# Optimization experiments

Measured on AMD Instinct MI355X. Metric: run time of the kernel, lower is better.

## Reference

```python
import jax, jax.numpy as jnp
import numpy as np

B, T, E, H, N_TAGS = 128, 512, 256, 512, 32
START, END = 30, 31


def setup_inputs() -> dict:
    key = jax.random.key(0)
    ks = jax.random.split(key, 12)
    s = 1.0 / np.sqrt(H)

    def w(k, shape):
        return jax.random.normal(k, shape, jnp.float32) * s

    X = jax.random.normal(ks[0], (B, T, E), jnp.float32)
    length = jnp.sort(jax.random.randint(ks[1], (B,), T // 2, T + 1))[::-1]
    masks = (jnp.arange(T)[None, :] < length[:, None]).astype(jnp.float32)
    W_ih_f, W_hh_f, b_f = w(ks[2], (4 * H, E)), w(ks[3], (4 * H, H)), w(ks[4], (4 * H,))
    W_ih_b, W_hh_b, b_b = w(ks[5], (4 * H, E)), w(ks[6], (4 * H, H)), w(ks[7], (4 * H,))
    W_out, b_out = w(ks[8], (N_TAGS, 2 * H)), w(ks[9], (N_TAGS,))
    transitions = jax.random.normal(ks[10], (N_TAGS, N_TAGS), jnp.float32)
    transitions = transitions.at[:, START].set(-1e4).at[END, :].set(-1e4)
    return dict(X=X, masks=masks, length=length,
                W_ih_f=W_ih_f, W_hh_f=W_hh_f, b_f=b_f,
                W_ih_b=W_ih_b, W_hh_b=W_hh_b, b_b=b_b,
                W_out=W_out, b_out=b_out, transitions=transitions)


def _lstm_dir(Xt, mt, Wih, Whh, b, reverse):
    # Xt: [T,B,E], mt: [T,B,1]. Masked update emulates pack_padded_sequence
    # (state frozen on pad; for reverse dir, state stays zero until last valid token).
    h0 = jnp.zeros((Xt.shape[1], H), Xt.dtype)

    def step(carry, inp):
        h, c = carry
        x, m = inp
        gates = x @ Wih.T + h @ Whh.T + b  # [B,4H], torch gate order i,f,g,o
        i, f, g, o = jnp.split(gates, 4, axis=-1)
        i, f, o = jax.nn.sigmoid(i), jax.nn.sigmoid(f), jax.nn.sigmoid(o)
        g = jnp.tanh(g)
        c_new = f * c + i * g
        h_new = o * jnp.tanh(c_new)
        h = m * h_new + (1.0 - m) * h
        c = m * c_new + (1.0 - m) * c
        return (h, c), h

    _, hs = jax.lax.scan(step, (h0, h0), (Xt, mt), reverse=reverse)
    return hs  # [T,B,H]


def reference(X, masks, length, W_ih_f, W_hh_f, b_f, W_ih_b, W_hh_b, b_b, W_out, b_out, transitions):
    Xt = X.transpose(1, 0, 2)            # [T,B,E]
    mT = masks.T                          # [T,B]
    mt = mT[:, :, None]
    hf = _lstm_dir(Xt, mt, W_ih_f, W_hh_f, b_f, False)
    hb = _lstm_dir(Xt, mt, W_ih_b, W_hh_b, b_b, True)
    emis = jnp.concatenate([hf, hb], axis=-1) @ W_out.T + b_out  # [T,B,n_tags]

    # Viterbi forward recurrence with masking
    alphas0 = emis[0] + transitions[START]  # [B,n]

    def vstep(alphas, inp):
        e, m = inp  # e: [B,n], m: [B,1]
        scores = alphas[:, :, None] + transitions[None] + e[:, None, :]  # [B,from,to]
        alphas = m * scores.max(axis=1) + (1.0 - m) * alphas
        return alphas, jnp.argmax(scores, axis=1)

    alphas, bps = jax.lax.scan(vstep, alphas0, (emis[1:], mt[1:]))
    final = alphas + transitions[:, END]
    max_end_scores = final.max(axis=1)      # [B]
    end_tags = jnp.argmax(final, axis=1)    # [B]

    # Masked backtrace: bps[k] is the backpointer into position k+1
    def bstep(cur, inp):
        bp, m = inp  # bp: [B,n], m: [B]
        prev = jnp.where(m > 0, jnp.take_along_axis(bp, cur[:, None], axis=1)[:, 0], cur)
        return prev, prev

    _, outs = jax.lax.scan(bstep, end_tags, (bps, mT[1:]), reverse=True)  # outs[k]=tag at pos k
    tags = jnp.concatenate([outs, end_tags[None]], axis=0).T              # [B,T]
    tags = jnp.where(masks > 0, tags, -1)
    return max_end_scores, tags
```

## Files before the change

kernel.cpp:

```cpp
#include <hip/hip_runtime.h>
#include <cfloat>
#include <cmath>

#define Bn 128
#define Tn 512
#define En 256
#define Hn 512
#define NTAGS 32

#define OFF_HF 0
#define OFF_HB 131072
#define OFF_CF 262144
#define OFF_CB 327680
#define OFF_EF 393216
#define OFF_EB 2490368

__global__ __launch_bounds__(512, 4) void lstm_step_k(
    const float* __restrict__ X, const float* __restrict__ masks,
    const float* __restrict__ Wih_f, const float* __restrict__ Whh_f, const float* __restrict__ bias_f,
    const float* __restrict__ Wih_b, const float* __restrict__ Whh_b, const float* __restrict__ bias_b,
    const float* __restrict__ Wout, float* __restrict__ ws, int s)
{
  __shared__ __align__(16) float P[8 * 8 * 128];
  __shared__ __align__(16) float GL[128 * 9];
  __shared__ __align__(16) float RS[8 * 128];

  const int tid  = threadIdx.x;
  const int blk  = blockIdx.x;
  const int lane = tid & 63;
  const int kq   = __builtin_amdgcn_readfirstlane(tid >> 6);
  const int bg   = lane & 31;
  const int kh   = lane >> 5;
  const int kloc = kq * 8 + kh * 4;

  const int dir = blk >> 8;
  const int bbk = blk & 255;
  const int t = dir ? (Tn - 1 - s) : s;
  const float* Wih  = dir ? Wih_b  : Wih_f;
  const float* Whh  = dir ? Whh_b  : Whh_f;
  const float* bias = dir ? bias_b : bias_f;
  float* hbuf = ws + (dir ? OFF_HB : OFF_HF);
  float* cbuf = ws + (dir ? OFF_CB : OFF_CF);
  const float* hprev = hbuf + ((s + 1) & 1) * (Hn * Bn);
  float*       hnext = hbuf + (s & 1) * (Hn * Bn);
  const int hidx0 = bbk * 2;
  const int etag  = bbk & 31;
  const int ebq   = bbk >> 5;

  const int pb  = tid & 127;
  const int phh = (tid >> 7) & 1;
  const int hidxp = hidx0 + phh;
  float mval = 0.f, bi = 0.f, bf_ = 0.f, bg_ = 0.f, bo_ = 0.f, cold = 0.f, hold = 0.f;
  if (tid < 256) {
    mval = masks[(size_t)pb * Tn + t];
    bi  = bias[hidxp];
    bf_ = bias[Hn + hidxp];
    bg_ = bias[2 * Hn + hidxp];
    bo_ = bias[3 * Hn + hidxp];
    cold = cbuf[hidxp * Bn + pb];
    hold = hprev[hidxp * Bn + pb];
  }

  const float* wor = Wout + (size_t)etag * (2 * Hn) + dir * Hn;

  float acc[4][8];
  #pragma unroll
  for (int m = 0; m < 4; ++m)
    #pragma unroll
    for (int n = 0; n < 8; ++n) acc[m][n] = 0.f;
  float eac[4] = {0.f, 0.f, 0.f, 0.f};

  #pragma unroll 1
  for (int c = 0; c < 8; ++c) {
    const int k0 = c * 64 + kloc;
    const float* ap = hprev + (size_t)k0 * Bn + bg * 4;
    const float4 A0 = *(const float4*)(ap);
    const float4 A1 = *(const float4*)(ap + Bn);
    const float4 A2 = *(const float4*)(ap + 2 * Bn);
    const float4 A3 = *(const float4*)(ap + 3 * Bn);
    float4 Wv[8];
    #pragma unroll
    for (int n = 0; n < 8; ++n) {
      const int cgl = (n >> 1) * Hn + hidx0 + (n & 1);
      Wv[n] = *(const float4*)(Whh + (size_t)cgl * Hn + k0);
    }
    const float4 wo4 = *(const float4*)(wor + k0);
    const float a0[4] = {A0.x, A0.y, A0.z, A0.w};
    const float a1[4] = {A1.x, A1.y, A1.z, A1.w};
    const float a2[4] = {A2.x, A2.y, A2.z, A2.w};
    const float a3[4] = {A3.x, A3.y, A3.z, A3.w};
    #pragma unroll
    for (int n = 0; n < 8; ++n) {
      const float w0 = Wv[n].x, w1 = Wv[n].y, w2 = Wv[n].z, w3 = Wv[n].w;
      #pragma unroll
      for (int m = 0; m < 4; ++m) {
        acc[m][n] += a0[m] * w0;
        acc[m][n] += a1[m] * w1;
        acc[m][n] += a2[m] * w2;
        acc[m][n] += a3[m] * w3;
      }
    }
    #pragma unroll
    for (int m = 0; m < 4; ++m) {
      eac[m] += a0[m] * wo4.x;
      eac[m] += a1[m] * wo4.y;
      eac[m] += a2[m] * wo4.z;
      eac[m] += a3[m] * wo4.w;
    }
  }

  #pragma unroll 1
  for (int c = 0; c < 4; ++c) {
    const int e0 = c * 64 + kloc;
    const float* xp = X + (size_t)(bg * 4) * (Tn * En) + (size_t)t * En + e0;
    const float4 X0 = *(const float4*)(xp);
    const float4 X1 = *(const float4*)(xp + Tn * En);
    const float4 X2 = *(const float4*)(xp + 2 * (Tn * En));
    const float4 X3 = *(const float4*)(xp + 3 * (Tn * En));
    float4 Wv[8];
    #pragma unroll
    for (int n = 0; n < 8; ++n) {
      const int cgl = (n >> 1) * Hn + hidx0 + (n & 1);
      Wv[n] = *(const float4*)(Wih + (size_t)cgl * En + e0);
    }
    #pragma unroll
    for (int n = 0; n < 8; ++n) {
      const float w0 = Wv[n].x, w1 = Wv[n].y, w2 = Wv[n].z, w3 = Wv[n].w;
      acc[0][n] += X0.x * w0; acc[0][n] += X0.y * w1; acc[0][n] += X0.z * w2; acc[0][n] += X0.w * w3;
      acc[1][n] += X1.x * w0; acc[1][n] += X1.y * w1; acc[1][n] += X1.z * w2; acc[1][n] += X1.w * w3;
      acc[2][n] += X2.x * w0; acc[2][n] += X2.y * w1; acc[2][n] += X2.z * w2; acc[2][n] += X2.w * w3;
      acc[3][n] += X3.x * w0; acc[3][n] += X3.y * w1; acc[3][n] += X3.z * w2; acc[3][n] += X3.w * w3;
    }
  }

  #pragma unroll
  for (int m = 0; m < 4; ++m)
    #pragma unroll
    for (int n = 0; n < 8; ++n)
      acc[m][n] += __shfl_xor(acc[m][n], 32);
  #pragma unroll
  for (int m = 0; m < 4; ++m) eac[m] += __shfl_xor(eac[m], 32);

  if (kh == 0) {
    #pragma unroll
    for (int n = 0; n < 8; ++n)
      *(float4*)&P[(kq * 8 + n) * 128 + bg * 4] =
          make_float4(acc[0][n], acc[1][n], acc[2][n], acc[3][n]);
    *(float4*)&RS[kq * 128 + bg * 4] = make_float4(eac[0], eac[1], eac[2], eac[3]);
  }
  __syncthreads();
  {
    const int b  = tid & 127;
    const int nq = tid >> 7;
    #pragma unroll
    for (int nn = 0; nn < 2; ++nn) {
      const int n = nq * 2 + nn;
      float v = 0.f;
      #pragma unroll
      for (int k2 = 0; k2 < 8; ++k2)
        v += P[(k2 * 8 + n) * 128 + b];
      GL[b * 9 + n] = v;
    }
  }
  if (s > 0 && ebq == 0 && tid < 128) {
    const int tprev = dir ? (Tn - s) : (s - 1);
    float* Edst = ws + (dir ? OFF_EB : OFF_EF);
    float v = 0.f;
    #pragma unroll
    for (int g = 0; g < 8; ++g) v += RS[g * 128 + tid];
    Edst[(size_t)tprev * (NTAGS * Bn) + etag * Bn + tid] = v;
  }
  __syncthreads();

  if (tid < 256) {
    const float gi = GL[pb * 9 + 0 + phh] + bi;
    const float gf = GL[pb * 9 + 2 + phh] + bf_;
    const float gc = GL[pb * 9 + 4 + phh] + bg_;
    const float go = GL[pb * 9 + 6 + phh] + bo_;
    const float iv = 1.f / (1.f + expf(-gi));
    const float fv = 1.f / (1.f + expf(-gf));
    const float gv = tanhf(gc);
    const float ov = 1.f / (1.f + expf(-go));
    const float cnew = fv * cold + iv * gv;
    const float hnew = ov * tanhf(cnew);
    hnext[hidxp * Bn + pb] = (mval > 0.f) ? hnew : hold;
    cbuf[hidxp * Bn + pb]  = (mval > 0.f) ? cnew : cold;
  }
}

__global__ __launch_bounds__(512) void emis_final_k(const float* __restrict__ Wout,
                                                    float* __restrict__ ws)
{
  __shared__ float RSf[16 * Bn];
  const int tid = threadIdx.x;
  const int dir = blockIdx.x >> 5;
  const int tag = blockIdx.x & 31;
  const float* hsrc = ws + (dir ? OFF_HB : OFF_HF) + 1 * (Hn * Bn);
  const int tprev = dir ? 0 : (Tn - 1);
  const float* wrow = Wout + (size_t)tag * (2 * Hn) + dir * Hn;
  float* Edst = ws + (dir ? OFF_EB : OFF_EF);
  const int bq = tid & 31;
  const int kg = tid >> 5;
  float4 a4 = make_float4(0.f, 0.f, 0.f, 0.f);
  #pragma unroll 4
  for (int kk = 0; kk < 32; ++kk) {
    const int k = kg * 32 + kk;
    const float w = wrow[k];
    const float4 h4 = *(const float4*)&hsrc[k * Bn + bq * 4];
    a4.x += h4.x * w; a4.y += h4.y * w; a4.z += h4.z * w; a4.w += h4.w * w;
  }
  *(float4*)&RSf[kg * Bn + bq * 4] = a4;
  __syncthreads();
  if (tid < 128) {
    float v = 0.f;
    #pragma unroll
    for (int g = 0; g < 16; ++g) v += RSf[g * Bn + tid];
    Edst[(size_t)tprev * (NTAGS * Bn) + tag * Bn + tid] = v;
  }
}

__global__ __launch_bounds__(64) void viterbi_k(
    const float* __restrict__ Ef, const float* __restrict__ Eb,
    const float* __restrict__ bout, const float* __restrict__ trans,
    const float* __restrict__ masks, float* __restrict__ out)
{
  const int b = blockIdx.x;
  const int l = threadIdx.x;
  __shared__ float tr[32][32];
  __shared__ float al[32];
  __shared__ float msk[512];
  __shared__ unsigned char bp[512][32];
  __shared__ int tseq[512];

  for (int i = l; i < 1024; i += 64) tr[i >> 5][i & 31] = trans[i];
  for (int i = l; i < 512; i += 64) msk[i] = masks[(size_t)b * 512 + i];
  __syncthreads();

  const int j  = l & 31;
  const int hi = l >> 5;
  if (l < 32)
    al[j] = Ef[(size_t)j * Bn + b] + Eb[(size_t)j * Bn + b] + bout[j] + tr[30][j];
  __syncthreads();

  for (int t = 1; t < 512; ++t) {
    float pmax = -FLT_MAX; int pidx = 0;
    #pragma unroll
    for (int ii = 0; ii < 16; ++ii) {
      const int i = hi * 16 + ii;
      const float sc = al[i] + tr[i][j];
      if (sc > pmax) { pmax = sc; pidx = i; }
    }
    const float omax = __shfl_down(pmax, 32);
    const int   oidx = __shfl_down(pidx, 32);
    if (l < 32) {
      if (omax > pmax) { pmax = omax; pidx = oidx; }
      bp[t][j] = (unsigned char)pidx;
      const float e = Ef[(size_t)t * (NTAGS * Bn) + j * Bn + b]
                    + Eb[(size_t)t * (NTAGS * Bn) + j * Bn + b] + bout[j];
      const float na = pmax + e;
      if (msk[t] > 0.f) al[j] = na;
    }
    __syncthreads();
  }

  float fv; int fidx;
  if (l < 32) { fv = al[l] + tr[l][31]; fidx = l; }
  else        { fv = -FLT_MAX; fidx = 1 << 30; }
  #pragma unroll
  for (int off = 16; off >= 1; off >>= 1) {
    const float v2 = __shfl_xor(fv, off);
    const int   i2 = __shfl_xor(fidx, off);
    if (v2 > fv || (v2 == fv && i2 < fidx)) { fv = v2; fidx = i2; }
  }
  if (l == 0) {
    out[b] = fv;
    int cur = fidx;
    tseq[511] = cur;
    for (int t = 511; t >= 1; --t) {
      const int prev = (msk[t] > 0.f) ? (int)bp[t][cur] : cur;
      tseq[t - 1] = prev;
      cur = prev;
    }
  }
  __syncthreads();
  for (int t = l; t < 512; t += 64) {
    const float tv = (msk[t] > 0.f) ? (float)tseq[t] : -1.0f;
    out[Bn + (size_t)b * 512 + t] = tv;
  }
}

extern "C" void kernel_launch(void* const* d_in, const int* in_sizes, int n_in,
                              void* d_out, int out_size, void* d_ws, size_t ws_size,
                              hipStream_t stream) {
  const float* X      = (const float*)d_in[0];
  const float* masks  = (const float*)d_in[1];
  const float* Wih_f  = (const float*)d_in[3];
  const float* Whh_f  = (const float*)d_in[4];
  const float* bf     = (const float*)d_in[5];
  const float* Wih_b  = (const float*)d_in[6];
  const float* Whh_b  = (const float*)d_in[7];
  const float* bb     = (const float*)d_in[8];
  const float* Wout   = (const float*)d_in[9];
  const float* bout   = (const float*)d_in[10];
  const float* trans  = (const float*)d_in[11];
  float* ws  = (float*)d_ws;
  float* out = (float*)d_out;

  hipMemsetAsync(d_ws, 0, (size_t)OFF_EF * sizeof(float), stream);

  for (int s = 0; s < Tn; ++s)
    lstm_step_k<<<512, 512, 0, stream>>>(X, masks, Wih_f, Whh_f, bf,
                                         Wih_b, Whh_b, bb, Wout, ws, s);
  emis_final_k<<<64, 512, 0, stream>>>(Wout, ws);
  viterbi_k<<<128, 64, 0, stream>>>(ws + OFF_EF, ws + OFF_EB, bout, trans, masks, out);
}
```

Measured before the change: 14.08 ms.

## Pre-transpose LSTM weights into gate-interleaved layout and halve step grid

Adds a one-time kernel that transposes Whh and Wih into a k-major layout with the four gates of each hidden unit interleaved, so each step reads 16 contiguous gate weights per k. The per-step kernel now handles 4 hidden units per block across 256 blocks (instead of 2 units across 512), with each thread doing a 2-batch by 16-column micro-tile over single k values. The intent is more coalesced weight reads, fewer blocks per launch and more reuse of each loaded h value. The costs are an extra transpose pass, more workspace, and launch bounds dropped to 2 blocks per SM, which lowers occupancy.

Measured after the change: 14.82 ms. +5.3%, slower.

```diff
diff --git a/kernel.cpp b/kernel.cpp
--- a/kernel.cpp
+++ b/kernel.cpp
@@ -14,169 +14,162 @@
 #define OFF_CB 327680
 #define OFF_EF 393216
 #define OFF_EB 2490368
-
-__global__ __launch_bounds__(512, 4) void lstm_step_k(
+#define OFF_WTG 4587520
+
+__global__ __launch_bounds__(512) void transpose_w_k(
+    const float* __restrict__ Wih_f, const float* __restrict__ Whh_f,
+    const float* __restrict__ Wih_b, const float* __restrict__ Whh_b,
+    float* __restrict__ ws)
+{
+  const int dir = blockIdx.x >> 10;
+  const int k   = blockIdx.x & 1023;
+  if (k >= 768) return;
+  const float* Whh = dir ? Whh_b : Whh_f;
+  const float* Wih = dir ? Wih_b : Wih_f;
+  float* outr = ws + OFF_WTG + ((size_t)dir * 768 + k) * 2048;
+  #pragma unroll
+  for (int i = 0; i < 4; ++i) {
+    const int cp = threadIdx.x + i * 512;
+    const int h = cp >> 2;
+    const int g = cp & 3;
+    outr[cp] = (k < Hn) ? Whh[(size_t)(g * Hn + h) * Hn + k]
+                        : Wih[(size_t)(g * Hn + h) * En + (k - Hn)];
+  }
+}
+
+__global__ __launch_bounds__(512, 2) void lstm_step_k(
     const float* __restrict__ X, const float* __restrict__ masks,
-    const float* __restrict__ Wih_f, const float* __restrict__ Whh_f, const float* __restrict__ bias_f,
-    const float* __restrict__ Wih_b, const float* __restrict__ Whh_b, const float* __restrict__ bias_b,
+    const float* __restrict__ bias_f, const float* __restrict__ bias_b,
     const float* __restrict__ Wout, float* __restrict__ ws, int s)
 {
-  __shared__ __align__(16) float P[8 * 8 * 128];
-  __shared__ __align__(16) float GL[128 * 9];
+  __shared__ __align__(16) float P[8 * 16 * 128];
+  __shared__ __align__(16) float GL[128 * 17];
   __shared__ __align__(16) float RS[8 * 128];
 
   const int tid  = threadIdx.x;
   const int blk  = blockIdx.x;
   const int lane = tid & 63;
   const int kq   = __builtin_amdgcn_readfirstlane(tid >> 6);
-  const int bg   = lane & 31;
-  const int kh   = lane >> 5;
-  const int kloc = kq * 8 + kh * 4;
-
-  const int dir = blk >> 8;
-  const int bbk = blk & 255;
+  const int b0   = lane * 2;
+
+  const int dir = blk >> 7;
+  const int bbk = blk & 127;
   const int t = dir ? (Tn - 1 - s) : s;
-  const float* Wih  = dir ? Wih_b  : Wih_f;
-  const float* Whh  = dir ? Whh_b  : Whh_f;
   const float* bias = dir ? bias_b : bias_f;
   float* hbuf = ws + (dir ? OFF_HB : OFF_HF);
   float* cbuf = ws + (dir ? OFF_CB : OFF_CF);
   const float* hprev = hbuf + ((s + 1) & 1) * (Hn * Bn);
   float*       hnext = hbuf + (s & 1) * (Hn * Bn);
-  const int hidx0 = bbk * 2;
+  const int hidx0 = bbk * 4;
   const int etag  = bbk & 31;
   const int ebq   = bbk >> 5;
 
   const int pb  = tid & 127;
-  const int phh = (tid >> 7) & 1;
+  const int phh = tid >> 7;
   const int hidxp = hidx0 + phh;
-  float mval = 0.f, bi = 0.f, bf_ = 0.f, bg_ = 0.f, bo_ = 0.f, cold = 0.f, hold = 0.f;
-  if (tid < 256) {
-    mval = masks[(size_t)pb * Tn + t];
-    bi  = bias[hidxp];
-    bf_ = bias[Hn + hidxp];
-    bg_ = bias[2 * Hn + hidxp];
-    bo_ = bias[3 * Hn + hidxp];
-    cold = cbuf[hidxp * Bn + pb];
-    hold = hprev[hidxp * Bn + pb];
-  }
-
-  const float* wor = Wout + (size_t)etag * (2 * Hn) + dir * Hn;
-
-  float acc[4][8];
+  const float mval = masks[(size_t)pb * Tn + t];
+  const float bi  = bias[hidxp];
+  const float bf_ = bias[Hn + hidxp];
+  const float bg_ = bias[2 * Hn + hidxp];
+  const float bo_ = bias[3 * Hn + hidxp];
+  const float cold = cbuf[hidxp * Bn + pb];
+  const float hold = hprev[hidxp * Bn + pb];
+
+  const float* WT  = ws + OFF_WTG + (size_t)dir * (768 * 2048) + hidx0 * 4;
+  const float* wox = Wout + (size_t)etag * (2 * Hn) + dir * Hn;
+
+  float acc[2][16];
   #pragma unroll
-  for (int m = 0; m < 4; ++m)
-    #pragma unroll
-    for (int n = 0; n < 8; ++n) acc[m][n] = 0.f;
-  float eac[4] = {0.f, 0.f, 0.f, 0.f};
-
-  #pragma unroll 1
+  for (int m = 0; m < 2; ++m)
+    #pragma unroll
+    for (int n = 0; n < 16; ++n) acc[m][n] = 0.f;
+  float eac[2] = {0.f, 0.f};
+
+  #pragma unroll 2
   for (int c = 0; c < 8; ++c) {
-    const int k0 = c * 64 + kloc;
-    const float* ap = hprev + (size_t)k0 * Bn + bg * 4;
-    const float4 A0 = *(const float4*)(ap);
-    const float4 A1 = *(const float4*)(ap + Bn);
-    const float4 A2 = *(const float4*)(ap + 2 * Bn);
-    const float4 A3 = *(const float4*)(ap + 3 * Bn);
-    float4 Wv[8];
-    #pragma unroll
-    for (int n = 0; n < 8; ++n) {
-      const int cgl = (n >> 1) * Hn + hidx0 + (n & 1);
-      Wv[n] = *(const float4*)(Whh + (size_t)cgl * Hn + k0);
-    }
-    const float4 wo4 = *(const float4*)(wor + k0);
-    const float a0[4] = {A0.x, A0.y, A0.z, A0.w};
-    const float a1[4] = {A1.x, A1.y, A1.z, A1.w};
-    const float a2[4] = {A2.x, A2.y, A2.z, A2.w};
-    const float a3[4] = {A3.x, A3.y, A3.z, A3.w};
-    #pragma unroll
-    for (int n = 0; n < 8; ++n) {
-      const float w0 = Wv[n].x, w1 = Wv[n].y, w2 = Wv[n].z, w3 = Wv[n].w;
+    const int kb = c * 64 + kq * 8;
+    #pragma unroll
+    for (int j = 0; j < 8; ++j) {
+      const int k = kb + j;
+      const float2 a  = *(const float2*)&hprev[(size_t)k * Bn + b0];
+      const float4 w0 = *(const float4*)(WT + (size_t)k * 2048);
+      const float4 w1 = *(const float4*)(WT + (size_t)k * 2048 + 4);
+      const float4 w2 = *(const float4*)(WT + (size_t)k * 2048 + 8);
+      const float4 w3 = *(const float4*)(WT + (size_t)k * 2048 + 12);
+      const float wo = wox[k];
+      const float w_[16] = {w0.x, w0.y, w0.z, w0.w, w1.x, w1.y, w1.z, w1.w,
+                            w2.x, w2.y, w2.z, w2.w, w3.x, w3.y, w3.z, w3.w};
       #pragma unroll
-      for (int m = 0; m < 4; ++m) {
-        acc[m][n] += a0[m] * w0;
-        acc[m][n] += a1[m] * w1;
-        acc[m][n] += a2[m] * w2;
-        acc[m][n] += a3[m] * w3;
+      for (int n = 0; n < 16; ++n) {
+        acc[0][n] += a.x * w_[n];
+        acc[1][n] += a.y * w_[n];
       }
-    }
-    #pragma unroll
-    for (int m = 0; m < 4; ++m) {
-      eac[m] += a0[m] * wo4.x;
-      eac[m] += a1[m] * wo4.y;
-      eac[m] += a2[m] * wo4.z;
-      eac[m] += a3[m] * wo4.w;
-    }
-  }
-
+      eac[0] += a.x * wo;
+      eac[1] += a.y * wo;
+    }
+  }
+
+  const size_t xrow0 = (size_t)b0 * (Tn * En) + (size_t)t * En;
+  const size_t xrow1 = xrow0 + (size_t)(Tn * En);
   #pragma unroll 1
   for (int c = 0; c < 4; ++c) {
-    const int e0 = c * 64 + kloc;
-    const float* xp = X + (size_t)(bg * 4) * (Tn * En) + (size_t)t * En + e0;
-    const float4 X0 = *(const float4*)(xp);
-    const float4 X1 = *(const float4*)(xp + Tn * En);
-    const float4 X2 = *(const float4*)(xp + 2 * (Tn * En));
-    const float4 X3 = *(const float4*)(xp + 3 * (Tn * En));
-    float4 Wv[8];
-    #pragma unroll
-    for (int n = 0; n < 8; ++n) {
-      const int cgl = (n >> 1) * Hn + hidx0 + (n & 1);
-      Wv[n] = *(const float4*)(Wih + (size_t)cgl * En + e0);
-    }
-    #pragma unroll
-    for (int n = 0; n < 8; ++n) {
-      const float w0 = Wv[n].x, w1 = Wv[n].y, w2 = Wv[n].z, w3 = Wv[n].w;
-      acc[0][n] += X0.x * w0; acc[0][n] += X0.y * w1; acc[0][n] += X0.z * w2; acc[0][n] += X0.w * w3;
-      acc[1][n] += X1.x * w0; acc[1][n] += X1.y * w1; acc[1][n] += X1.z * w2; acc[1][n] += X1.w * w3;
-      acc[2][n] += X2.x * w0; acc[2][n] += X2.y * w1; acc[2][n] += X2.z * w2; acc[2][n] += X2.w * w3;
-      acc[3][n] += X3.x * w0; acc[3][n] += X3.y * w1; acc[3][n] += X3.z * w2; acc[3][n] += X3.w * w3;
+    const int e0 = c * 64 + kq * 8;
+    const float4 xa0 = *(const float4*)&X[xrow0 + e0];
+    const float4 xa1 = *(const float4*)&X[xrow0 + e0 + 4];
+    const float4 xb0 = *(const float4*)&X[xrow1 + e0];
+    const float4 xb1 = *(const float4*)&X[xrow1 + e0 + 4];
+    const float x0[8] = {xa0.x, xa0.y, xa0.z, xa0.w, xa1.x, xa1.y, xa1.z, xa1.w};
+    const float x1[8] = {xb0.x, xb0.y, xb0.z, xb0.w, xb1.x, xb1.y, xb1.z, xb1.w};
+    #pragma unroll
+    for (int j = 0; j < 8; ++j) {
+      const int k = 512 + e0 + j;
+      const float4 w0 = *(const float4*)(WT + (size_t)k * 2048);
+      const float4 w1 = *(const float4*)(WT + (size_t)k * 2048 + 4);
+      const float4 w2 = *(const float4*)(WT + (size_t)k * 2048 + 8);
+      const float4 w3 = *(const float4*)(WT + (size_t)k * 2048 + 12);
+      const float w_[16] = {w0.x, w0.y, w0.z, w0.w, w1.x, w1.y, w1.z, w1.w,
+                            w2.x, w2.y, w2.z, w2.w, w3.x, w3.y, w3.z, w3.w};
+      #pragma unroll
+      for (int n = 0; n < 16; ++n) {
+        acc[0][n] += x0[j] * w_[n];
+        acc[1][n] += x1[j] * w_[n];
+      }
     }
   }
 
   #pragma unroll
-  for (int m = 0; m < 4; ++m)
-    #pragma unroll
-    for (int n = 0; n < 8; ++n)
-      acc[m][n] += __shfl_xor(acc[m][n], 32);
-  #pragma unroll
-  for (int m = 0; m < 4; ++m) eac[m] += __shfl_xor(eac[m], 32);
-
-  if (kh == 0) {
-    #pragma unroll
-    for (int n = 0; n < 8; ++n)
-      *(float4*)&P[(kq * 8 + n) * 128 + bg * 4] =
-          make_float4(acc[0][n], acc[1][n], acc[2][n], acc[3][n]);
-    *(float4*)&RS[kq * 128 + bg * 4] = make_float4(eac[0], eac[1], eac[2], eac[3]);
-  }
+  for (int n = 0; n < 16; ++n)
+    *(float2*)&P[(kq * 16 + n) * 128 + b0] = make_float2(acc[0][n], acc[1][n]);
+  *(float2*)&RS[kq * 128 + b0] = make_float2(eac[0], eac[1]);
   __syncthreads();
   {
     const int b  = tid & 127;
     const int nq = tid >> 7;
     #pragma unroll
-    for (int nn = 0; nn < 2; ++nn) {
-      const int n = nq * 2 + nn;
+    for (int nn = 0; nn < 4; ++nn) {
+      const int n = nq * 4 + nn;
       float v = 0.f;
       #pragma unroll
       for (int k2 = 0; k2 < 8; ++k2)
-        v += P[(k2 * 8 + n) * 128 + b];
-      GL[b * 9 + n] = v;
-    }
-  }
-  if (s > 0 && ebq == 0 && tid < 128) {
+        v += P[(k2 * 16 + n) * 128 + b];
+      GL[b * 17 + n] = v;
+    }
+  }
+  if (s > 0 && tid < 32) {
     const int tprev = dir ? (Tn - s) : (s - 1);
     float* Edst = ws + (dir ? OFF_EB : OFF_EF);
     float v = 0.f;
     #pragma unroll
-    for (int g = 0; g < 8; ++g) v += RS[g * 128 + tid];
-    Edst[(size_t)tprev * (NTAGS * Bn) + etag * Bn + tid] = v;
-  }
-  __syncthreads();
-
-  if (tid < 256) {
-    const float gi = GL[pb * 9 + 0 + phh] + bi;
-    const float gf = GL[pb * 9 + 2 + phh] + bf_;
-    const float gc = GL[pb * 9 + 4 + phh] + bg_;
-    const float go = GL[pb * 9 + 6 + phh] + bo_;
+    for (int g = 0; g < 8; ++g) v += RS[g * 128 + ebq * 32 + tid];
+    Edst[(size_t)tprev * (NTAGS * Bn) + etag * Bn + ebq * 32 + tid] = v;
+  }
+  __syncthreads();
+
+  {
+    const float gi = GL[pb * 17 + phh * 4 + 0] + bi;
+    const float gf = GL[pb * 17 + phh * 4 + 1] + bf_;
+    const float gc = GL[pb * 17 + phh * 4 + 2] + bg_;
+    const float go = GL[pb * 17 + phh * 4 + 3] + bo_;
     const float iv = 1.f / (1.f + expf(-gi));
     const float fv = 1.f / (1.f + expf(-gf));
     const float gv = tanhf(gc);
@@ -308,9 +301,10 @@
 
   hipMemsetAsync(d_ws, 0, (size_t)OFF_EF * sizeof(float), stream);
 
+  transpose_w_k<<<2048, 512, 0, stream>>>(Wih_f, Whh_f, Wih_b, Whh_b, ws);
+
   for (int s = 0; s < Tn; ++s)
-    lstm_step_k<<<512, 512, 0, stream>>>(X, masks, Wih_f, Whh_f, bf,
-                                         Wih_b, Whh_b, bb, Wout, ws, s);
+    lstm_step_k<<<256, 512, 0, stream>>>(X, masks, bf, bb, Wout, ws, s);
   emis_final_k<<<64, 512, 0, stream>>>(Wout, ws);
   viterbi_k<<<128, 64, 0, stream>>>(ws + OFF_EF, ws + OFF_EB, bout, trans, masks, out);
 }
```
